# Kernel tuning notes

Hardware: AMD Instinct MI355X
Metric: run time of the kernel (lower is better)

The kernel has to match this reference:

```python
import jax, jax.numpy as jnp
import numpy as np

N_NODES = 50000   # gates in the circuit batch
N_HOPS = 100000   # number of k-hop cones
MAX_PI = 8        # max PIs per hop (padded, masked via stats == -1)
D = 128           # token_emb / hidden
D_FF = 4 * D      # cls_head hidden width (512)
TT = 64           # max_tt_len -> logits width
LN_EPS = 1e-5


def setup_inputs() -> dict:
    key = jax.random.key(0)
    ks = jax.random.split(key, 8)
    hf = jax.random.normal(ks[0], (N_NODES, D), jnp.float32)
    all_hop_pi = jax.random.randint(ks[1], (N_HOPS, MAX_PI), 0, N_NODES)
    # stats in {-1, 0, 1}; -1 marks an invalid (padded) PI slot
    all_hop_pi_stats = jax.random.randint(ks[2], (N_HOPS, MAX_PI), 0, 3) - 1
    all_hop_po = jax.random.randint(ks[3], (N_HOPS,), 0, N_NODES)
    w_q = jax.random.normal(ks[4], (D,), jnp.float32) / np.sqrt(D)
    W1 = jax.random.normal(ks[5], (D, D_FF), jnp.float32) / np.sqrt(D)
    b1 = jnp.zeros((D_FF,), jnp.float32)
    gamma = jnp.ones((D_FF,), jnp.float32)
    beta = jnp.zeros((D_FF,), jnp.float32)
    W2 = jax.random.normal(ks[6], (D_FF, TT), jnp.float32) / np.sqrt(D_FF)
    b2 = jnp.zeros((TT,), jnp.float32)
    return {
        'hf': hf, 'w_q': w_q, 'W1': W1, 'b1': b1, 'gamma': gamma,
        'beta': beta, 'W2': W2, 'b2': b2,
        'all_hop_pi': all_hop_pi, 'all_hop_pi_stats': all_hop_pi_stats,
        'all_hop_po': all_hop_po,
    }


def reference(hf, w_q, W1, b1, gamma, beta, W2, b2,
              all_hop_pi, all_hop_pi_stats, all_hop_po):
    # Per-hop gather: valid PI embeddings + PO embedding -> [H, P+1, D]
    pi_tok = hf[all_hop_pi]                       # [H, P, D]
    po_tok = hf[all_hop_po][:, None, :]           # [H, 1, D]
    tokens = jnp.concatenate([pi_tok, po_tok], axis=1)
    valid = jnp.concatenate(
        [all_hop_pi_stats != -1,
         jnp.ones((all_hop_po.shape[0], 1), bool)], axis=1)  # [H, P+1]
    # tf_Pooling: masked single-query attention pooling over the ragged set
    scores = jnp.einsum('hpd,d->hp', tokens, w_q) / jnp.sqrt(jnp.float32(D))
    scores = jnp.where(valid, scores, jnp.float32(-1e30))
    attn = jax.nn.softmax(scores, axis=-1)
    hop_hf = jnp.einsum('hp,hpd->hd', attn, tokens)  # [H, D]
    # cls_head: Linear(D, 4D) -> ReLU -> LayerNorm(4D) -> Linear(4D, TT)
    h = jax.nn.relu(hop_hf @ W1 + b1)
    mu = jnp.mean(h, axis=-1, keepdims=True)
    var = jnp.var(h, axis=-1, keepdims=True)
    h = (h - mu) * jax.lax.rsqrt(var + LN_EPS) * gamma + beta
    logits = h @ W2 + b2                           # [H, TT]
    return logits
```

## Files before the change

### kernel.cpp

```cpp
#include <hip/hip_runtime.h>
#include <hip/hip_bf16.h>
#include <math.h>

#define DIM 128
#define DFF 512
#define TTW 64
#define NPI 8
#define NTOK 9
#define TILE_H 32

typedef __attribute__((ext_vector_type(8))) short short8;
typedef __attribute__((ext_vector_type(4))) float float4v;

__device__ __forceinline__ float bf16lo_f32(unsigned u) {
    union { unsigned u; float f; } v; v.u = u << 16;
    return v.f;
}
__device__ __forceinline__ float bf16hi_f32(unsigned u) {
    union { unsigned u; float f; } v; v.u = u & 0xffff0000u;
    return v.f;
}
__device__ __forceinline__ unsigned pk_bf16(float a, float b) {
    __hip_bfloat162 h = __float22bfloat162_rn(float2{a, b});
    union { __hip_bfloat162 h; unsigned u; } cv; cv.h = h;
    return cv.u;
}

__global__ __launch_bounds__(256)
void prep_k(const float* __restrict__ hf, const float* __restrict__ W1,
            const float* __restrict__ W2,
            unsigned short* __restrict__ hf2, unsigned short* __restrict__ w1t,
            unsigned short* __restrict__ w2t,
            int n_hf, int B_HF)
{
    __shared__ float tile[32][33];
    const int b = blockIdx.x, t = threadIdx.x;
    if (b < B_HF) {
        int i = (b * 256 + t) * 8;
        if (i < n_hf) {
            float4v v0 = *(const float4v*)(hf + i);
            float4v v1 = *(const float4v*)(hf + i + 4);
            uint4 o;
            o.x = pk_bf16(v0[0], v0[1]);
            o.y = pk_bf16(v0[2], v0[3]);
            o.z = pk_bf16(v1[0], v1[1]);
            o.w = pk_bf16(v1[2], v1[3]);
            *(uint4*)(hf2 + i) = o;
        }
    } else if (b < B_HF + 64) {
        const int tb = b - B_HF;
        const int r0 = (tb & 3) * 32, c0 = (tb >> 2) * 32;
        const int ty = t >> 3, tx = t & 7;
        *(float4v*)&tile[ty][tx * 4] = *(const float4v*)(W1 + (r0 + ty) * DFF + c0 + tx * 4);
        __syncthreads();
        uint2 o;
        o.x = pk_bf16(tile[tx * 4 + 0][ty], tile[tx * 4 + 1][ty]);
        o.y = pk_bf16(tile[tx * 4 + 2][ty], tile[tx * 4 + 3][ty]);
        *(uint2*)(w1t + (c0 + ty) * DIM + r0 + tx * 4) = o;
    } else {
        const int tb = b - B_HF - 64;
        const int r0 = (tb & 15) * 32, c0 = (tb >> 4) * 32;
        const int ty = t >> 3, tx = t & 7;
        *(float4v*)&tile[ty][tx * 4] = *(const float4v*)(W2 + (r0 + ty) * TTW + c0 + tx * 4);
        __syncthreads();
        uint2 o;
        o.x = pk_bf16(tile[tx * 4 + 0][ty], tile[tx * 4 + 1][ty]);
        o.y = pk_bf16(tile[tx * 4 + 2][ty], tile[tx * 4 + 3][ty]);
        *(uint2*)(w2t + (c0 + ty) * DFF + r0 + tx * 4) = o;
    }
}

__global__ __launch_bounds__(256, 3)
void fused_k(const unsigned short* __restrict__ hf2,
             const float* __restrict__ w_q,
             const int* __restrict__ pi,
             const int* __restrict__ stats,
             const int* __restrict__ po,
             const unsigned short* __restrict__ w1t,
             const float* __restrict__ b1,
             const float* __restrict__ gamma,
             const float* __restrict__ beta,
             const unsigned short* __restrict__ w2t,
             const float* __restrict__ b2,
             float* __restrict__ out,
             int H)
{
    __shared__ __align__(16) unsigned short Hsm[TILE_H][DFF + 8];
    __shared__ float part[2][16][4][2];
    unsigned short (*Apool)[DIM + 8] = (unsigned short (*)[DIM + 8])&Hsm[0][0];

    const int t    = threadIdx.x;
    const int lane = t & 63;
    const int w    = t >> 6;
    const int row  = lane & 15;
    const int quad = lane >> 4;
    const int hop0 = blockIdx.x * TILE_H;

    {
        const int g = t >> 5, l = t & 31;
        const float4v wq4 = *(const float4v*)(w_q + l * 4);
        #pragma unroll
        for (int it = 0; it < 4; ++it) {
            const int hl = g + it * 8;
            const int hop = hop0 + hl;
            uint2 o = {0u, 0u};
            if (hop < H) {
                int idx[NTOK]; bool val[NTOK];
                int4 p0 = *(const int4*)(pi + hop * NPI);
                int4 p1 = *(const int4*)(pi + hop * NPI + 4);
                int4 s0 = *(const int4*)(stats + hop * NPI);
                int4 s1 = *(const int4*)(stats + hop * NPI + 4);
                idx[0]=p0.x; val[0]=s0.x != -1;
                idx[1]=p0.y; val[1]=s0.y != -1;
                idx[2]=p0.z; val[2]=s0.z != -1;
                idx[3]=p0.w; val[3]=s0.w != -1;
                idx[4]=p1.x; val[4]=s1.x != -1;
                idx[5]=p1.y; val[5]=s1.y != -1;
                idx[6]=p1.z; val[6]=s1.z != -1;
                idx[7]=p1.w; val[7]=s1.w != -1;
                idx[8]=po[hop]; val[8]=true;
                uint2 tu[NTOK];
                #pragma unroll
                for (int p = 0; p < NTOK; ++p)
                    tu[p] = *(const uint2*)(hf2 + (size_t)idx[p] * DIM + l * 4);
                float tok[NTOK][4];
                #pragma unroll
                for (int p = 0; p < NTOK; ++p) {
                    tok[p][0] = bf16lo_f32(tu[p].x);
                    tok[p][1] = bf16hi_f32(tu[p].x);
                    tok[p][2] = bf16lo_f32(tu[p].y);
                    tok[p][3] = bf16hi_f32(tu[p].y);
                }
                float sc[NTOK];
                #pragma unroll
                for (int p = 0; p < NTOK; ++p)
                    sc[p] = tok[p][0]*wq4[0] + tok[p][1]*wq4[1]
                          + tok[p][2]*wq4[2] + tok[p][3]*wq4[3];
                #pragma unroll
                for (int m = 1; m < 32; m <<= 1) {
                    #pragma unroll
                    for (int p = 0; p < NTOK; ++p) sc[p] += __shfl_xor(sc[p], m);
                }
                const float isd = 0.08838834764831845f;
                float mx = -1e30f;
                #pragma unroll
                for (int p = 0; p < NTOK; ++p) {
                    sc[p] = val[p] ? sc[p] * isd : -1e30f;
                    mx = fmaxf(mx, sc[p]);
                }
                float se = 0.f;
                #pragma unroll
                for (int p = 0; p < NTOK; ++p) { sc[p] = __expf(sc[p] - mx); se += sc[p]; }
                const float inv = 1.f / se;
                float a0=0.f, a1=0.f, a2=0.f, a3=0.f;
                #pragma unroll
                for (int p = 0; p < NTOK; ++p) {
                    float a = sc[p] * inv;
                    a0 += a * tok[p][0]; a1 += a * tok[p][1];
                    a2 += a * tok[p][2]; a3 += a * tok[p][3];
                }
                o.x = pk_bf16(a0, a1);
                o.y = pk_bf16(a2, a3);
            }
            *(uint2*)&Apool[hl][l * 4] = o;
        }
    }
    __syncthreads();

    float4v acc[8][2];
    #pragma unroll
    for (int mt = 0; mt < 8; ++mt) {
        acc[mt][0] = (float4v){0.f, 0.f, 0.f, 0.f};
        acc[mt][1] = (float4v){0.f, 0.f, 0.f, 0.f};
    }
    {
        short8 bfr[2][4];
        #pragma unroll
        for (int ks = 0; ks < 4; ++ks) {
            const int k0 = ks * 32 + quad * 8;
            #pragma unroll
            for (int ht = 0; ht < 2; ++ht)
                bfr[ht][ks] = *(const short8*)&Apool[ht * 16 + row][k0];
        }
        #pragma unroll
        for (int mt = 0; mt < 8; ++mt) {
            const unsigned short* wrow = w1t + (size_t)(w * 128 + mt * 16 + row) * DIM;
            #pragma unroll
            for (int ks = 0; ks < 4; ++ks) {
                short8 afr = *(const short8*)(wrow + ks * 32 + quad * 8);
                acc[mt][0] = __builtin_amdgcn_mfma_f32_16x16x32_bf16(afr, bfr[0][ks], acc[mt][0], 0, 0, 0);
                acc[mt][1] = __builtin_amdgcn_mfma_f32_16x16x32_bf16(afr, bfr[1][ks], acc[mt][1], 0, 0, 0);
            }
        }
    }
    float sum0 = 0.f, ssq0 = 0.f, sum1 = 0.f, ssq1 = 0.f;
    #pragma unroll
    for (int mt = 0; mt < 8; ++mt) {
        const int nb = w * 128 + mt * 16 + quad * 4;
        const float4v bias = *(const float4v*)(b1 + nb);
        #pragma unroll
        for (int r = 0; r < 4; ++r) {
            float v0 = fmaxf(acc[mt][0][r] + bias[r], 0.f);
            float v1 = fmaxf(acc[mt][1][r] + bias[r], 0.f);
            acc[mt][0][r] = v0;  sum0 += v0;  ssq0 += v0 * v0;
            acc[mt][1][r] = v1;  sum1 += v1;  ssq1 += v1 * v1;
        }
    }
    #pragma unroll
    for (int m = 16; m <= 32; m <<= 1) {
        sum0 += __shfl_xor(sum0, m);  ssq0 += __shfl_xor(ssq0, m);
        sum1 += __shfl_xor(sum1, m);  ssq1 += __shfl_xor(ssq1, m);
    }
    if (lane < 16) {
        part[0][row][w][0] = sum0;  part[0][row][w][1] = ssq0;
        part[1][row][w][0] = sum1;  part[1][row][w][1] = ssq1;
    }
    __syncthreads();
    float mu[2], rs[2];
    #pragma unroll
    for (int ht = 0; ht < 2; ++ht) {
        float S = 0.f, Q = 0.f;
        #pragma unroll
        for (int ww = 0; ww < 4; ++ww) {
            S += part[ht][row][ww][0];
            Q += part[ht][row][ww][1];
        }
        const float invn = 1.f / (float)DFF;
        mu[ht] = S * invn;
        float var = Q * invn - mu[ht] * mu[ht];
        rs[ht] = rsqrtf(var + 1e-5f);
    }
    #pragma unroll
    for (int mt = 0; mt < 8; ++mt) {
        const int nb = w * 128 + mt * 16 + quad * 4;
        const float4v g4  = *(const float4v*)(gamma + nb);
        const float4v be4 = *(const float4v*)(beta + nb);
        #pragma unroll
        for (int ht = 0; ht < 2; ++ht) {
            float o[4];
            #pragma unroll
            for (int r = 0; r < 4; ++r) {
                float tg = rs[ht] * g4[r];
                o[r] = acc[mt][ht][r] * tg + (be4[r] - mu[ht] * tg);
            }
            uint2 p;
            p.x = pk_bf16(o[0], o[1]);
            p.y = pk_bf16(o[2], o[3]);
            *(uint2*)&Hsm[ht * 16 + row][nb] = p;
        }
    }
    __syncthreads();

    {
        float4v acc2[2];
        acc2[0] = (float4v){0.f,0.f,0.f,0.f};
        acc2[1] = (float4v){0.f,0.f,0.f,0.f};
        #pragma unroll
        for (int ks = 0; ks < 16; ++ks) {
            const int k0 = ks * 32 + quad * 8;
            short8 bfr = *(const short8*)(w2t + (size_t)(w * 16 + row) * DFF + k0);
            #pragma unroll
            for (int mt = 0; mt < 2; ++mt) {
                short8 afr = *(const short8*)&Hsm[mt * 16 + row][k0];
                acc2[mt] = __builtin_amdgcn_mfma_f32_16x16x32_bf16(
                    afr, bfr, acc2[mt], 0, 0, 0);
            }
        }
        const float bb = b2[w * 16 + row];
        #pragma unroll
        for (int mt = 0; mt < 2; ++mt) {
            #pragma unroll
            for (int r = 0; r < 4; ++r) {
                int hop = hop0 + mt * 16 + quad * 4 + r;
                if (hop < H)
                    out[(size_t)hop * TTW + w * 16 + row] = acc2[mt][r] + bb;
            }
        }
    }
}

extern "C" void kernel_launch(void* const* d_in, const int* in_sizes, int n_in,
                              void* d_out, int out_size, void* d_ws, size_t ws_size,
                              hipStream_t stream) {
    const float* hf    = (const float*)d_in[0];
    const float* w_q   = (const float*)d_in[1];
    const float* W1    = (const float*)d_in[2];
    const float* b1    = (const float*)d_in[3];
    const float* gamma = (const float*)d_in[4];
    const float* beta  = (const float*)d_in[5];
    const float* W2    = (const float*)d_in[6];
    const float* b2    = (const float*)d_in[7];
    const int* pi      = (const int*)d_in[8];
    const int* stats   = (const int*)d_in[9];
    const int* po      = (const int*)d_in[10];
    float* out         = (float*)d_out;

    const int n_hf = in_sizes[0];
    const int H    = in_sizes[10];

    char* ws = (char*)d_ws;
    unsigned short* w1t = (unsigned short*)ws;
    unsigned short* w2t = (unsigned short*)(ws + 131072);
    unsigned short* hf2 = (unsigned short*)(ws + 196608);

    const int B_HF = (n_hf + 2047) / 2048;
    const int prep_blocks = B_HF + 96;

    hipLaunchKernelGGL(prep_k, dim3(prep_blocks), dim3(256), 0, stream,
                       hf, W1, W2, hf2, w1t, w2t, n_hf, B_HF);
    hipLaunchKernelGGL(fused_k, dim3((H + TILE_H - 1) / TILE_H), dim3(256), 0, stream,
                       hf2, w_q, pi, stats, po, w1t, b1, gamma, beta, w2t, b2, out, H);
}
```

Before: 213.3 us.

## Merge weight prep into a persistent cooperative kernel with grid sync

Folds the bf16 conversion and transpose of hf, W1 and W2 into the main kernel, separated from the compute by a cooperative grid-wide sync. This removes the second kernel launch and the gap between the two launches. The kernel becomes persistent, looping over tiles, and the hop tile shrinks from 32 to 16 so each MFMA weight fragment is reused across half as many hops. It adds host-side occupancy and attribute queries on every call and risks grid-sync overhead, with a fallback to the old two-kernel path.

```diff
diff --git a/kernel.cpp b/kernel.cpp
--- a/kernel.cpp
+++ b/kernel.cpp
@@ -1,13 +1,16 @@
 #include <hip/hip_runtime.h>
 #include <hip/hip_bf16.h>
+#include <hip/hip_cooperative_groups.h>
 #include <math.h>
+
+namespace cg = cooperative_groups;
 
 #define DIM 128
 #define DFF 512
 #define TTW 64
 #define NPI 8
 #define NTOK 9
-#define TILE_H 32
+#define TILE_H 16
 
 typedef __attribute__((ext_vector_type(8))) short short8;
 typedef __attribute__((ext_vector_type(4))) float float4v;
@@ -70,212 +73,234 @@
     }
 }
 
+template<bool COOP>
 __global__ __launch_bounds__(256, 3)
-void fused_k(const unsigned short* __restrict__ hf2,
+void fused_t(const float* __restrict__ hf,
              const float* __restrict__ w_q,
              const int* __restrict__ pi,
              const int* __restrict__ stats,
              const int* __restrict__ po,
-             const unsigned short* __restrict__ w1t,
+             const float* __restrict__ W1,
+             const float* __restrict__ W2,
              const float* __restrict__ b1,
              const float* __restrict__ gamma,
              const float* __restrict__ beta,
-             const unsigned short* __restrict__ w2t,
              const float* __restrict__ b2,
+             unsigned short* __restrict__ hf2,
+             unsigned short* __restrict__ w1t,
+             unsigned short* __restrict__ w2t,
              float* __restrict__ out,
-             int H)
+             int H, int ntiles, int n_hf)
 {
     __shared__ __align__(16) unsigned short Hsm[TILE_H][DFF + 8];
-    __shared__ float part[2][16][4][2];
+    __shared__ float part[16][4][2];
     unsigned short (*Apool)[DIM + 8] = (unsigned short (*)[DIM + 8])&Hsm[0][0];
+    float (*tile)[33] = (float (*)[33])&Hsm[0][0];
 
     const int t    = threadIdx.x;
     const int lane = t & 63;
     const int w    = t >> 6;
     const int row  = lane & 15;
     const int quad = lane >> 4;
-    const int hop0 = blockIdx.x * TILE_H;
-
-    {
-        const int g = t >> 5, l = t & 31;
-        const float4v wq4 = *(const float4v*)(w_q + l * 4);
+
+    if constexpr (COOP) {
+        const int stride = gridDim.x * 256 * 8;
+        for (int i = (blockIdx.x * 256 + t) * 8; i < n_hf; i += stride) {
+            float4v v0 = *(const float4v*)(hf + i);
+            float4v v1 = *(const float4v*)(hf + i + 4);
+            uint4 o;
+            o.x = pk_bf16(v0[0], v0[1]);
+            o.y = pk_bf16(v0[2], v0[3]);
+            o.z = pk_bf16(v1[0], v1[1]);
+            o.w = pk_bf16(v1[2], v1[3]);
+            *(uint4*)(hf2 + i) = o;
+        }
+        if (blockIdx.x < 64) {
+            const int tb = blockIdx.x;
+            const int r0 = (tb & 3) * 32, c0 = (tb >> 2) * 32;
+            const int ty = t >> 3, tx = t & 7;
+            *(float4v*)&tile[ty][tx * 4] = *(const float4v*)(W1 + (r0 + ty) * DFF + c0 + tx * 4);
+            __syncthreads();
+            uint2 o;
+            o.x = pk_bf16(tile[tx * 4 + 0][ty], tile[tx * 4 + 1][ty]);
+            o.y = pk_bf16(tile[tx * 4 + 2][ty], tile[tx * 4 + 3][ty]);
+            *(uint2*)(w1t + (c0 + ty) * DIM + r0 + tx * 4) = o;
+        } else if (blockIdx.x < 96) {
+            const int tb = blockIdx.x - 64;
+            const int r0 = (tb & 15) * 32, c0 = (tb >> 4) * 32;
+            const int ty = t >> 3, tx = t & 7;
+            *(float4v*)&tile[ty][tx * 4] = *(const float4v*)(W2 + (r0 + ty) * TTW + c0 + tx * 4);
+            __syncthreads();
+            uint2 o;
+            o.x = pk_bf16(tile[tx * 4 + 0][ty], tile[tx * 4 + 1][ty]);
+            o.y = pk_bf16(tile[tx * 4 + 2][ty], tile[tx * 4 + 3][ty]);
+            *(uint2*)(w2t + (c0 + ty) * DFF + r0 + tx * 4) = o;
+        }
+        __threadfence();
+        cg::this_grid().sync();
+        __syncthreads();
+    }
+
+    for (int tilei = blockIdx.x; tilei < ntiles; tilei += gridDim.x) {
+        const int hop0 = tilei * TILE_H;
+
+        {
+            const int g = t >> 5, l = t & 31;
+            const float4v wq4 = *(const float4v*)(w_q + l * 4);
+            #pragma unroll
+            for (int it = 0; it < 2; ++it) {
+                const int hl = g + it * 8;
+                const int hop = hop0 + hl;
+                uint2 o = {0u, 0u};
+                if (hop < H) {
+                    int idx[NTOK]; bool val[NTOK];
+                    int4 p0 = *(const int4*)(pi + hop * NPI);
+                    int4 p1 = *(const int4*)(pi + hop * NPI + 4);
+                    int4 s0 = *(const int4*)(stats + hop * NPI);
+                    int4 s1 = *(const int4*)(stats + hop * NPI + 4);
+                    idx[0]=p0.x; val[0]=s0.x != -1;
+                    idx[1]=p0.y; val[1]=s0.y != -1;
+                    idx[2]=p0.z; val[2]=s0.z != -1;
+                    idx[3]=p0.w; val[3]=s0.w != -1;
+                    idx[4]=p1.x; val[4]=s1.x != -1;
+                    idx[5]=p1.y; val[5]=s1.y != -1;
+                    idx[6]=p1.z; val[6]=s1.z != -1;
+                    idx[7]=p1.w; val[7]=s1.w != -1;
+                    idx[8]=po[hop]; val[8]=true;
+                    uint2 tu[NTOK];
+                    #pragma unroll
+                    for (int p = 0; p < NTOK; ++p)
+                        tu[p] = *(const uint2*)(hf2 + (size_t)idx[p] * DIM + l * 4);
+                    float tok[NTOK][4];
+                    #pragma unroll
+                    for (int p = 0; p < NTOK; ++p) {
+                        tok[p][0] = bf16lo_f32(tu[p].x);
+                        tok[p][1] = bf16hi_f32(tu[p].x);
+                        tok[p][2] = bf16lo_f32(tu[p].y);
+                        tok[p][3] = bf16hi_f32(tu[p].y);
+                    }
+                    float sc[NTOK];
+                    #pragma unroll
+                    for (int p = 0; p < NTOK; ++p)
+                        sc[p] = tok[p][0]*wq4[0] + tok[p][1]*wq4[1]
+                              + tok[p][2]*wq4[2] + tok[p][3]*wq4[3];
+                    #pragma unroll
+                    for (int m = 1; m < 32; m <<= 1) {
+                        #pragma unroll
+                        for (int p = 0; p < NTOK; ++p) sc[p] += __shfl_xor(sc[p], m);
+                    }
+                    const float isd = 0.08838834764831845f;
+                    float mx = -1e30f;
+                    #pragma unroll
+                    for (int p = 0; p < NTOK; ++p) {
+                        sc[p] = val[p] ? sc[p] * isd : -1e30f;
+                        mx = fmaxf(mx, sc[p]);
+                    }
+                    float se = 0.f;
+                    #pragma unroll
+                    for (int p = 0; p < NTOK; ++p) { sc[p] = __expf(sc[p] - mx); se += sc[p]; }
+                    const float inv = 1.f / se;
+                    float a0=0.f, a1=0.f, a2=0.f, a3=0.f;
+                    #pragma unroll
+                    for (int p = 0; p < NTOK; ++p) {
+                        float a = sc[p] * inv;
+                        a0 += a * tok[p][0]; a1 += a * tok[p][1];
+                        a2 += a * tok[p][2]; a3 += a * tok[p][3];
+                    }
+                    o.x = pk_bf16(a0, a1);
+                    o.y = pk_bf16(a2, a3);
+                }
+                *(uint2*)&Apool[hl][l * 4] = o;
+            }
+        }
+        __syncthreads();
+
+        float4v acc[8];
         #pragma unroll
-        for (int it = 0; it < 4; ++it) {
-            const int hl = g + it * 8;
-            const int hop = hop0 + hl;
-            uint2 o = {0u, 0u};
-            if (hop < H) {
-                int idx[NTOK]; bool val[NTOK];
-                int4 p0 = *(const int4*)(pi + hop * NPI);
-                int4 p1 = *(const int4*)(pi + hop * NPI + 4);
-                int4 s0 = *(const int4*)(stats + hop * NPI);
-                int4 s1 = *(const int4*)(stats + hop * NPI + 4);
-                idx[0]=p0.x; val[0]=s0.x != -1;
-                idx[1]=p0.y; val[1]=s0.y != -1;
-                idx[2]=p0.z; val[2]=s0.z != -1;
-                idx[3]=p0.w; val[3]=s0.w != -1;
-                idx[4]=p1.x; val[4]=s1.x != -1;
-                idx[5]=p1.y; val[5]=s1.y != -1;
-                idx[6]=p1.z; val[6]=s1.z != -1;
-                idx[7]=p1.w; val[7]=s1.w != -1;
-                idx[8]=po[hop]; val[8]=true;
-                uint2 tu[NTOK];
+        for (int mt = 0; mt < 8; ++mt) acc[mt] = (float4v){0.f, 0.f, 0.f, 0.f};
+        {
+            short8 bfr[4];
+            #pragma unroll
+            for (int ks = 0; ks < 4; ++ks)
+                bfr[ks] = *(const short8*)&Apool[row][ks * 32 + quad * 8];
+            #pragma unroll
+            for (int mt = 0; mt < 8; ++mt) {
+                const unsigned short* wrow = w1t + (size_t)(w * 128 + mt * 16 + row) * DIM;
                 #pragma unroll
-                for (int p = 0; p < NTOK; ++p)
-                    tu[p] = *(const uint2*)(hf2 + (size_t)idx[p] * DIM + l * 4);
-                float tok[NTOK][4];
-                #pragma unroll
-                for (int p = 0; p < NTOK; ++p) {
-                    tok[p][0] = bf16lo_f32(tu[p].x);
-                    tok[p][1] = bf16hi_f32(tu[p].x);
-                    tok[p][2] = bf16lo_f32(tu[p].y);
-                    tok[p][3] = bf16hi_f32(tu[p].y);
+                for (int ks = 0; ks < 4; ++ks) {
+                    short8 afr = *(const short8*)(wrow + ks * 32 + quad * 8);
+                    acc[mt] = __builtin_amdgcn_mfma_f32_16x16x32_bf16(afr, bfr[ks], acc[mt], 0, 0, 0);
                 }
-                float sc[NTOK];
-                #pragma unroll
-                for (int p = 0; p < NTOK; ++p)
-                    sc[p] = tok[p][0]*wq4[0] + tok[p][1]*wq4[1]
-                          + tok[p][2]*wq4[2] + tok[p][3]*wq4[3];
-                #pragma unroll
-                for (int m = 1; m < 32; m <<= 1) {
-                    #pragma unroll
-                    for (int p = 0; p < NTOK; ++p) sc[p] += __shfl_xor(sc[p], m);
-                }
-                const float isd = 0.08838834764831845f;
-                float mx = -1e30f;
-                #pragma unroll
-                for (int p = 0; p < NTOK; ++p) {
-                    sc[p] = val[p] ? sc[p] * isd : -1e30f;
-                    mx = fmaxf(mx, sc[p]);
-                }
-                float se = 0.f;
-                #pragma unroll
-                for (int p = 0; p < NTOK; ++p) { sc[p] = __expf(sc[p] - mx); se += sc[p]; }
-                const float inv = 1.f / se;
-                float a0=0.f, a1=0.f, a2=0.f, a3=0.f;
-                #pragma unroll
-                for (int p = 0; p < NTOK; ++p) {
-                    float a = sc[p] * inv;
-                    a0 += a * tok[p][0]; a1 += a * tok[p][1];
-                    a2 += a * tok[p][2]; a3 += a * tok[p][3];
-                }
-                o.x = pk_bf16(a0, a1);
-                o.y = pk_bf16(a2, a3);
-            }
-            *(uint2*)&Apool[hl][l * 4] = o;
-        }
-    }
-    __syncthreads();
-
-    float4v acc[8][2];
-    #pragma unroll
-    for (int mt = 0; mt < 8; ++mt) {
-        acc[mt][0] = (float4v){0.f, 0.f, 0.f, 0.f};
-        acc[mt][1] = (float4v){0.f, 0.f, 0.f, 0.f};
-    }
-    {
-        short8 bfr[2][4];
-        #pragma unroll
-        for (int ks = 0; ks < 4; ++ks) {
-            const int k0 = ks * 32 + quad * 8;
-            #pragma unroll
-            for (int ht = 0; ht < 2; ++ht)
-                bfr[ht][ks] = *(const short8*)&Apool[ht * 16 + row][k0];
-        }
+            }
+        }
+        float sum0 = 0.f, ssq0 = 0.f;
         #pragma unroll
         for (int mt = 0; mt < 8; ++mt) {
-            const unsigned short* wrow = w1t + (size_t)(w * 128 + mt * 16 + row) * DIM;
-            #pragma unroll
-            for (int ks = 0; ks < 4; ++ks) {
-                short8 afr = *(const short8*)(wrow + ks * 32 + quad * 8);
-                acc[mt][0] = __builtin_amdgcn_mfma_f32_16x16x32_bf16(afr, bfr[0][ks], acc[mt][0], 0, 0, 0);
-                acc[mt][1] = __builtin_amdgcn_mfma_f32_16x16x32_bf16(afr, bfr[1][ks], acc[mt][1], 0, 0, 0);
-            }
-        }
-    }
-    float sum0 = 0.f, ssq0 = 0.f, sum1 = 0.f, ssq1 = 0.f;
-    #pragma unroll
-    for (int mt = 0; mt < 8; ++mt) {
-        const int nb = w * 128 + mt * 16 + quad * 4;
-        const float4v bias = *(const float4v*)(b1 + nb);
+            const int nb = w * 128 + mt * 16 + quad * 4;
+            const float4v bias = *(const float4v*)(b1 + nb);
+            #pragma unroll
+            for (int r = 0; r < 4; ++r) {
+                float v0 = fmaxf(acc[mt][r] + bias[r], 0.f);
+                acc[mt][r] = v0;  sum0 += v0;  ssq0 += v0 * v0;
+            }
+        }
         #pragma unroll
-        for (int r = 0; r < 4; ++r) {
-            float v0 = fmaxf(acc[mt][0][r] + bias[r], 0.f);
-            float v1 = fmaxf(acc[mt][1][r] + bias[r], 0.f);
-            acc[mt][0][r] = v0;  sum0 += v0;  ssq0 += v0 * v0;
-            acc[mt][1][r] = v1;  sum1 += v1;  ssq1 += v1 * v1;
-        }
-    }
-    #pragma unroll
-    for (int m = 16; m <= 32; m <<= 1) {
-        sum0 += __shfl_xor(sum0, m);  ssq0 += __shfl_xor(ssq0, m);
-        sum1 += __shfl_xor(sum1, m);  ssq1 += __shfl_xor(ssq1, m);
-    }
-    if (lane < 16) {
-        part[0][row][w][0] = sum0;  part[0][row][w][1] = ssq0;
-        part[1][row][w][0] = sum1;  part[1][row][w][1] = ssq1;
-    }
-    __syncthreads();
-    float mu[2], rs[2];
-    #pragma unroll
-    for (int ht = 0; ht < 2; ++ht) {
-        float S = 0.f, Q = 0.f;
+        for (int m = 16; m <= 32; m <<= 1) {
+            sum0 += __shfl_xor(sum0, m);  ssq0 += __shfl_xor(ssq0, m);
+        }
+        if (lane < 16) {
+            part[row][w][0] = sum0;  part[row][w][1] = ssq0;
+        }
+        __syncthreads();
+        float mu, rs;
+        {
+            float S = 0.f, Q = 0.f;
+            #pragma unroll
+            for (int ww = 0; ww < 4; ++ww) {
+                S += part[row][ww][0];
+                Q += part[row][ww][1];
+            }
+            const float invn = 1.f / (float)DFF;
+            mu = S * invn;
+            float var = Q * invn - mu * mu;
+            rs = rsqrtf(var + 1e-5f);
+        }
         #pragma unroll
-        for (int ww = 0; ww < 4; ++ww) {
-            S += part[ht][row][ww][0];
-            Q += part[ht][row][ww][1];
-        }
-        const float invn = 1.f / (float)DFF;
-        mu[ht] = S * invn;
-        float var = Q * invn - mu[ht] * mu[ht];
-        rs[ht] = rsqrtf(var + 1e-5f);
-    }
-    #pragma unroll
-    for (int mt = 0; mt < 8; ++mt) {
-        const int nb = w * 128 + mt * 16 + quad * 4;
-        const float4v g4  = *(const float4v*)(gamma + nb);
-        const float4v be4 = *(const float4v*)(beta + nb);
-        #pragma unroll
-        for (int ht = 0; ht < 2; ++ht) {
+        for (int mt = 0; mt < 8; ++mt) {
+            const int nb = w * 128 + mt * 16 + quad * 4;
+            const float4v g4  = *(const float4v*)(gamma + nb);
+            const float4v be4 = *(const float4v*)(beta + nb);
             float o[4];
             #pragma unroll
             for (int r = 0; r < 4; ++r) {
-                float tg = rs[ht] * g4[r];
-                o[r] = acc[mt][ht][r] * tg + (be4[r] - mu[ht] * tg);
+                float tg = rs * g4[r];
+                o[r] = acc[mt][r] * tg + (be4[r] - mu * tg);
             }
             uint2 p;
             p.x = pk_bf16(o[0], o[1]);
             p.y = pk_bf16(o[2], o[3]);
-            *(uint2*)&Hsm[ht * 16 + row][nb] = p;
-        }
-    }
-    __syncthreads();
-
-    {
-        float4v acc2[2];
-        acc2[0] = (float4v){0.f,0.f,0.f,0.f};
-        acc2[1] = (float4v){0.f,0.f,0.f,0.f};
-        #pragma unroll
-        for (int ks = 0; ks < 16; ++ks) {
-            const int k0 = ks * 32 + quad * 8;
-            short8 bfr = *(const short8*)(w2t + (size_t)(w * 16 + row) * DFF + k0);
-            #pragma unroll
-            for (int mt = 0; mt < 2; ++mt) {
-                short8 afr = *(const short8*)&Hsm[mt * 16 + row][k0];
-                acc2[mt] = __builtin_amdgcn_mfma_f32_16x16x32_bf16(
-                    afr, bfr, acc2[mt], 0, 0, 0);
-            }
-        }
-        const float bb = b2[w * 16 + row];
-        #pragma unroll
-        for (int mt = 0; mt < 2; ++mt) {
+            *(uint2*)&Hsm[row][nb] = p;
+        }
+        __syncthreads();
+
+        {
+            float4v acc2 = (float4v){0.f,0.f,0.f,0.f};
+            #pragma unroll
+            for (int ks = 0; ks < 16; ++ks) {
+                const int k0 = ks * 32 + quad * 8;
+                short8 bfr = *(const short8*)(w2t + (size_t)(w * 16 + row) * DFF + k0);
+                short8 afr = *(const short8*)&Hsm[row][k0];
+                acc2 = __builtin_amdgcn_mfma_f32_16x16x32_bf16(afr, bfr, acc2, 0, 0, 0);
+            }
+            const float bb = b2[w * 16 + row];
             #pragma unroll
             for (int r = 0; r < 4; ++r) {
-                int hop = hop0 + mt * 16 + quad * 4 + r;
+                int hop = hop0 + quad * 4 + r;
                 if (hop < H)
-                    out[(size_t)hop * TTW + w * 16 + row] = acc2[mt][r] + bb;
-            }
-        }
+                    out[(size_t)hop * TTW + w * 16 + row] = acc2[r] + bb;
+            }
+        }
+        __syncthreads();
     }
 }
 
@@ -295,19 +320,41 @@
     const int* po      = (const int*)d_in[10];
     float* out         = (float*)d_out;
 
-    const int n_hf = in_sizes[0];
-    const int H    = in_sizes[10];
+    int n_hf = in_sizes[0];
+    int H    = in_sizes[10];
+    int ntiles = (H + TILE_H - 1) / TILE_H;
 
     char* ws = (char*)d_ws;
     unsigned short* w1t = (unsigned short*)ws;
     unsigned short* w2t = (unsigned short*)(ws + 131072);
     unsigned short* hf2 = (unsigned short*)(ws + 196608);
 
+    int coop_attr = 0, dev = 0;
+    hipGetDevice(&dev);
+    hipDeviceGetAttribute(&coop_attr, hipDeviceAttributeCooperativeLaunch, dev);
+    int maxb = 0;
+    hipError_t oe = hipOccupancyMaxActiveBlocksPerMultiprocessor(
+        &maxb, fused_t<true>, 256, 0);
+
+    if (coop_attr && oe == hipSuccess && maxb >= 2) {
+        int grid = 256 * maxb;
+        if (grid > 2048) grid = 2048;
+        void* args[] = {
+            (void*)&hf, (void*)&w_q, (void*)&pi, (void*)&stats, (void*)&po,
+            (void*)&W1, (void*)&W2, (void*)&b1, (void*)&gamma, (void*)&beta,
+            (void*)&b2, (void*)&hf2, (void*)&w1t, (void*)&w2t, (void*)&out,
+            (void*)&H, (void*)&ntiles, (void*)&n_hf
+        };
+        hipError_t le = hipLaunchCooperativeKernel((const void*)&fused_t<true>,
+                                                   dim3(grid), dim3(256),
+                                                   args, 0, stream);
+        if (le == hipSuccess) return;
+    }
+
     const int B_HF = (n_hf + 2047) / 2048;
-    const int prep_blocks = B_HF + 96;
-
-    hipLaunchKernelGGL(prep_k, dim3(prep_blocks), dim3(256), 0, stream,
+    hipLaunchKernelGGL(prep_k, dim3(B_HF + 96), dim3(256), 0, stream,
                        hf, W1, W2, hf2, w1t, w2t, n_hf, B_HF);
-    hipLaunchKernelGGL(fused_k, dim3((H + TILE_H - 1) / TILE_H), dim3(256), 0, stream,
-                       hf2, w_q, pi, stats, po, w1t, b1, gamma, beta, w2t, b2, out, H);
-}
+    hipLaunchKernelGGL((fused_t<false>), dim3(ntiles), dim3(256), 0, stream,
+                       hf, w_q, pi, stats, po, W1, W2, b1, gamma, beta, b2,
+                       hf2, w1t, w2t, out, H, ntiles, n_hf);
+}
```

Measured after the change: 670.8 us. 3.14x slower.
